# Performance work log

Hardware: AMD Instinct MI355X
Metric: run time of the kernel (lower is better)

The kernel has to match this reference:

```python
import jax, jax.numpy as jnp
import numpy as np

E = 8          # num_tasks / experts (world_size=1 -> local_experts=E)
N = 8192       # tokens
H = 768        # hidden_size
I = 3072       # intermediate_size
EPS = 1e-12    # layer_norm_eps


def setup_inputs() -> dict:
    key = jax.random.key(0)
    ks = jax.random.split(key, 8)
    x = jax.random.normal(ks[0], (N, H), dtype=jnp.float32)
    # arange task ids -> hash (mod E) gives perfectly balanced expert loads
    task_ids = jnp.arange(N, dtype=jnp.int64)
    s1 = 1.0 / np.sqrt(H)
    s2 = 1.0 / np.sqrt(I)
    W1 = jax.random.uniform(ks[1], (E, H, I), jnp.float32, -s1, s1)
    b1 = jax.random.uniform(ks[2], (E, I), jnp.float32, -s1, s1)
    W2 = jax.random.uniform(ks[3], (E, I, H), jnp.float32, -s2, s2)
    b2 = jax.random.uniform(ks[4], (E, H), jnp.float32, -s2, s2)
    gamma = jnp.ones((E, H), jnp.float32)
    beta = jnp.zeros((E, H), jnp.float32)
    return {"x": x, "task_ids": task_ids, "W1": W1, "b1": b1,
            "W2": W2, "b2": b2, "gamma": gamma, "beta": beta}


def reference(x, task_ids, W1, b1, W2, b2, gamma, beta):
    # hash protocol: expert = task_id % num_experts
    expert = (task_ids % E).astype(jnp.int32)
    order = jnp.argsort(expert)              # dispatch (scatter router)
    C = N // E                               # balanced capacity per expert
    xs = x[order].reshape(E, C, H)           # [E, C, H] per-expert token blocks
    # per-expert FFN as grouped GEMMs
    h = jnp.einsum('ech,ehi->eci', xs, W1) + b1[:, None, :]
    h = jax.nn.gelu(h, approximate=False)
    y = jnp.einsum('eci,eih->ech', h, W2) + b2[:, None, :]
    # dropout is identity in eval; residual + per-expert LayerNorm
    z = y + xs
    mu = jnp.mean(z, axis=-1, keepdims=True)
    var = jnp.mean((z - mu) ** 2, axis=-1, keepdims=True)
    z = (z - mu) * jax.lax.rsqrt(var + EPS)
    z = z * gamma[:, None, :] + beta[:, None, :]
    # combine (gather router): undo the dispatch permutation
    out = jnp.zeros((N, H), x.dtype).at[order].set(z.reshape(N, H))
    return out
```

## Files before the change

kernel.cpp:

```cpp
#include <hip/hip_runtime.h>
#include <hip/hip_bf16.h>

#define NE   8
#define NTOK 8192
#define DH   768
#define DI   3072
#define CAP  1024

typedef __bf16 bf16x8 __attribute__((ext_vector_type(8)));
typedef float  f32x4  __attribute__((ext_vector_type(4)));

__device__ __forceinline__ void gload_lds16(const void* g, void* l) {
  __builtin_amdgcn_global_load_lds(
      (const __attribute__((address_space(1))) unsigned int*)g,
      (__attribute__((address_space(3))) unsigned int*)l, 16, 0, 0);
}

__global__ __launch_bounds__(256)
void transpose_cvt(const float* __restrict__ in, __hip_bfloat16* __restrict__ out,
                   int R, int C) {
  __shared__ float tile[32][33];
  const int e = blockIdx.z;
  const float* src = in + (size_t)e * R * C;
  __hip_bfloat16* dst = out + (size_t)e * R * C;
  const int c0 = blockIdx.x * 32, r0 = blockIdx.y * 32;
  const int tx = threadIdx.x, ty = threadIdx.y;
#pragma unroll
  for (int j = 0; j < 4; ++j)
    tile[ty + 8 * j][tx] = src[(size_t)(r0 + ty + 8 * j) * C + c0 + tx];
  __syncthreads();
#pragma unroll
  for (int j = 0; j < 4; ++j)
    dst[(size_t)(c0 + ty + 8 * j) * R + r0 + tx] = __float2bfloat16(tile[tx][ty + 8 * j]);
}

__global__ __launch_bounds__(256)
void gather_cvt_x(const float* __restrict__ x, __hip_bfloat16* __restrict__ xs) {
  const int j = blockIdx.x * 256 + threadIdx.x;
  const int orow = j / 96;
  const int k8 = (j - orow * 96) * 8;
  const int e = orow >> 10, c = orow & 1023;
  const int tok = c * 8 + e;
  const float4* p = (const float4*)(x + (size_t)tok * DH + k8);
  float4 u = p[0], v = p[1];
  __hip_bfloat16 tmp[8];
  tmp[0] = __float2bfloat16(u.x); tmp[1] = __float2bfloat16(u.y);
  tmp[2] = __float2bfloat16(u.z); tmp[3] = __float2bfloat16(u.w);
  tmp[4] = __float2bfloat16(v.x); tmp[5] = __float2bfloat16(v.y);
  tmp[6] = __float2bfloat16(v.z); tmp[7] = __float2bfloat16(v.w);
  *(uint4*)(xs + (size_t)orow * DH + k8) = *(const uint4*)tmp;
}

template <int EPI>
__global__ __launch_bounds__(256)
void gemm_bt(const __hip_bfloat16* __restrict__ A,
             const __hip_bfloat16* __restrict__ Bt,
             const float* __restrict__ bias,
             void* __restrict__ OutP,
             int N, int K, int NK,
             size_t sAe, size_t sBe, size_t sOe, int sBias) {
  __shared__ __hip_bfloat16 As[128 * 64];
  __shared__ __hip_bfloat16 Bs[128 * 64];

  const int t = threadIdx.x;
  const int lane = t & 63;
  const int w = t >> 6;
  const int g = lane >> 4;
  const int l15 = lane & 15;
  const int wm = w >> 1, wn = w & 1;
  const int e = blockIdx.z;

  const __hip_bfloat16* Ae = A + (size_t)e * sAe + (size_t)blockIdx.y * 128 * K;
  const __hip_bfloat16* Be = Bt + (size_t)e * sBe + (size_t)blockIdx.x * 128 * K;

  const int rowStg = t >> 3;
  const int srcOff = ((t & 7) ^ (rowStg & 7)) * 8;
  const size_t stgBase = (size_t)rowStg * K + srcOff;

  f32x4 acc[4][4] = {};

  for (int kt = 0; kt < NK; ++kt) {
    const int k0 = kt * 64;
#pragma unroll
    for (int i = 0; i < 4; ++i) {
      gload_lds16(Ae + stgBase + (size_t)i * 32 * K + k0, (char*)As + (i * 256 + t) * 16);
      gload_lds16(Be + stgBase + (size_t)i * 32 * K + k0, (char*)Bs + (i * 256 + t) * 16);
    }
    __syncthreads();
#pragma unroll
    for (int ks = 0; ks < 2; ++ks) {
      bf16x8 af[4], bv[4];
#pragma unroll
      for (int fm = 0; fm < 4; ++fm) {
        const int r = wm * 64 + fm * 16 + l15;
        af[fm] = *(const bf16x8*)((const char*)As + r * 128 + ((ks * 4 + g) ^ (r & 7)) * 16);
      }
#pragma unroll
      for (int fn = 0; fn < 4; ++fn) {
        const int r = wn * 64 + fn * 16 + l15;
        bv[fn] = *(const bf16x8*)((const char*)Bs + r * 128 + ((ks * 4 + g) ^ (r & 7)) * 16);
      }
#pragma unroll
      for (int fm = 0; fm < 4; ++fm)
#pragma unroll
        for (int fn = 0; fn < 4; ++fn)
          acc[fm][fn] = __builtin_amdgcn_mfma_f32_16x16x32_bf16(af[fm], bv[fn], acc[fm][fn], 0, 0, 0);
    }
    __syncthreads();
  }

  const float* biasE = bias + (size_t)e * sBias + blockIdx.x * 128;
  if (EPI == 0) {
    __hip_bfloat16* O = (__hip_bfloat16*)OutP + (size_t)e * sOe +
                        (size_t)blockIdx.y * 128 * N + blockIdx.x * 128;
#pragma unroll
    for (int fm = 0; fm < 4; ++fm)
#pragma unroll
      for (int fn = 0; fn < 4; ++fn) {
        const int n = wn * 64 + fn * 16 + l15;
        const float bvv = biasE[n];
#pragma unroll
        for (int r = 0; r < 4; ++r) {
          const int m = wm * 64 + fm * 16 + g * 4 + r;
          float v = acc[fm][fn][r] + bvv;
          v = 0.5f * v * (1.0f + erff(v * 0.70710678118654752f));
          O[(size_t)m * N + n] = __float2bfloat16(v);
        }
      }
  } else {
    float* O = (float*)OutP + (size_t)e * sOe +
               (size_t)blockIdx.y * 128 * N + blockIdx.x * 128;
#pragma unroll
    for (int fm = 0; fm < 4; ++fm)
#pragma unroll
      for (int fn = 0; fn < 4; ++fn) {
        const int n = wn * 64 + fn * 16 + l15;
        const float bvv = biasE[n];
#pragma unroll
        for (int r = 0; r < 4; ++r) {
          const int m = wm * 64 + fm * 16 + g * 4 + r;
          O[(size_t)m * N + n] = acc[fm][fn][r] + bvv;
        }
      }
  }
}

__global__ __launch_bounds__(256)
void resid_ln(const float* __restrict__ y, const float* __restrict__ x,
              const float* __restrict__ gamma, const float* __restrict__ beta,
              float* __restrict__ out) {
  const int row = blockIdx.x;
  const int e = row >> 10, c = row & 1023;
  const int tok = c * 8 + e;
  const float* yr = y + (size_t)row * DH;
  const float* xr = x + (size_t)tok * DH;
  const int t = threadIdx.x;
  float z[3];
  float s = 0.f, s2 = 0.f;
#pragma unroll
  for (int j = 0; j < 3; ++j) {
    const float v = yr[t + 256 * j] + xr[t + 256 * j];
    z[j] = v; s += v; s2 += v * v;
  }
#pragma unroll
  for (int off = 32; off; off >>= 1) {
    s += __shfl_down(s, off);
    s2 += __shfl_down(s2, off);
  }
  __shared__ float rs[4], rs2[4];
  if ((t & 63) == 0) { rs[t >> 6] = s; rs2[t >> 6] = s2; }
  __syncthreads();
  const float S = rs[0] + rs[1] + rs[2] + rs[3];
  const float S2 = rs2[0] + rs2[1] + rs2[2] + rs2[3];
  const float mu = S * (1.0f / DH);
  const float var = S2 * (1.0f / DH) - mu * mu;
  const float rstd = rsqrtf(var + 1e-12f);
  const float* ga = gamma + (size_t)e * DH;
  const float* be = beta + (size_t)e * DH;
  float* orow = out + (size_t)tok * DH;
#pragma unroll
  for (int j = 0; j < 3; ++j) {
    const int h = t + 256 * j;
    orow[h] = (z[j] - mu) * rstd * ga[h] + be[h];
  }
}

extern "C" void kernel_launch(void* const* d_in, const int* in_sizes, int n_in,
                              void* d_out, int out_size, void* d_ws, size_t ws_size,
                              hipStream_t stream) {
  const float* x     = (const float*)d_in[0];
  const float* W1    = (const float*)d_in[2];
  const float* b1    = (const float*)d_in[3];
  const float* W2    = (const float*)d_in[4];
  const float* b2    = (const float*)d_in[5];
  const float* gamma = (const float*)d_in[6];
  const float* beta  = (const float*)d_in[7];
  float* out = (float*)d_out;

  __hip_bfloat16* W1t = (__hip_bfloat16*)d_ws;
  __hip_bfloat16* W2t = W1t + (size_t)NE * DH * DI;
  __hip_bfloat16* hbuf = W2t + (size_t)NE * DH * DI;
  __hip_bfloat16* xs = hbuf + (size_t)NTOK * DI;
  float* ybuf = (float*)xs;

  dim3 tb(32, 8);
  transpose_cvt<<<dim3(DI / 32, DH / 32, NE), tb, 0, stream>>>(W1, W1t, DH, DI);
  transpose_cvt<<<dim3(DH / 32, DI / 32, NE), tb, 0, stream>>>(W2, W2t, DI, DH);
  gather_cvt_x<<<(NTOK * (DH / 8)) / 256, 256, 0, stream>>>(x, xs);

  gemm_bt<0><<<dim3(DI / 128, CAP / 128, NE), 256, 0, stream>>>(
      xs, W1t, b1, hbuf, DI, DH, DH / 64,
      (size_t)CAP * DH, (size_t)DI * DH, (size_t)CAP * DI, DI);

  gemm_bt<1><<<dim3(DH / 128, CAP / 128, NE), 256, 0, stream>>>(
      hbuf, W2t, b2, ybuf, DH, DI, DI / 64,
      (size_t)CAP * DI, (size_t)DH * DI, (size_t)CAP * DH, DH);

  resid_ln<<<NTOK, 256, 0, stream>>>(ybuf, x, gamma, beta, out);
}
```

Measured before the change: 358.3 us.

## Split-K second GEMM, XCD-aware block remap, and vectorized swizzled weight transpose

```diff
diff --git a/kernel.cpp b/kernel.cpp
--- a/kernel.cpp
+++ b/kernel.cpp
@@ -19,19 +19,40 @@
 __global__ __launch_bounds__(256)
 void transpose_cvt(const float* __restrict__ in, __hip_bfloat16* __restrict__ out,
                    int R, int C) {
-  __shared__ float tile[32][33];
+  __shared__ float lds[64 * 64];
   const int e = blockIdx.z;
   const float* src = in + (size_t)e * R * C;
   __hip_bfloat16* dst = out + (size_t)e * R * C;
-  const int c0 = blockIdx.x * 32, r0 = blockIdx.y * 32;
-  const int tx = threadIdx.x, ty = threadIdx.y;
-#pragma unroll
-  for (int j = 0; j < 4; ++j)
-    tile[ty + 8 * j][tx] = src[(size_t)(r0 + ty + 8 * j) * C + c0 + tx];
+  const int c0 = blockIdx.x * 64, r0 = blockIdx.y * 64;
+  const int t = threadIdx.x;
+
+  {
+    const int rr = t >> 4;
+    const int cq = t & 15;
+#pragma unroll
+    for (int j = 0; j < 4; ++j) {
+      const int r = rr + 16 * j;
+      const float4 v = *(const float4*)(src + (size_t)(r0 + r) * C + c0 + cq * 4);
+      *(float4*)&lds[r * 64 + ((cq ^ ((r >> 3) & 7)) << 2)] = v;
+    }
+  }
   __syncthreads();
-#pragma unroll
-  for (int j = 0; j < 4; ++j)
-    dst[(size_t)(c0 + ty + 8 * j) * R + r0 + tx] = __float2bfloat16(tile[tx][ty + 8 * j]);
+  {
+    const int r8 = (t & 7) * 8;
+    const int cb = t >> 3;
+#pragma unroll
+    for (int j = 0; j < 2; ++j) {
+      const int c = cb + 32 * j;
+      __hip_bfloat16 tmp[8];
+#pragma unroll
+      for (int i = 0; i < 8; ++i) {
+        const int rr = r8 + i;
+        tmp[i] = __float2bfloat16(
+            lds[rr * 64 + ((((c >> 2) ^ ((rr >> 3) & 7)) << 2) | (c & 3))]);
+      }
+      *(uint4*)(dst + (size_t)(c0 + c) * R + r0 + r8) = *(const uint4*)tmp;
+    }
+  }
 }
 
 __global__ __launch_bounds__(256)
@@ -57,10 +78,21 @@
              const __hip_bfloat16* __restrict__ Bt,
              const float* __restrict__ bias,
              void* __restrict__ OutP,
-             int N, int K, int NK,
-             size_t sAe, size_t sBe, size_t sOe, int sBias) {
+             int N, int K, int KK, int gx, int gy, int nsplit,
+             size_t sAe, size_t sBe, size_t sOe, int sBias, size_t sSplit) {
   __shared__ __hip_bfloat16 As[128 * 64];
   __shared__ __hip_bfloat16 Bs[128 * 64];
+
+  const int nblk = gridDim.x;
+  const int chunk = nblk >> 3;
+  const int id = (blockIdx.x & 7) * chunk + (blockIdx.x >> 3);
+  const int per_e = gx * gy * nsplit;
+  const int e = id / per_e;
+  int r = id - e * per_e;
+  const int s = r / (gx * gy);
+  r -= s * (gx * gy);
+  const int bx = r / gy;
+  const int by = r - bx * gy;
 
   const int t = threadIdx.x;
   const int lane = t & 63;
@@ -68,10 +100,9 @@
   const int g = lane >> 4;
   const int l15 = lane & 15;
   const int wm = w >> 1, wn = w & 1;
-  const int e = blockIdx.z;
-
-  const __hip_bfloat16* Ae = A + (size_t)e * sAe + (size_t)blockIdx.y * 128 * K;
-  const __hip_bfloat16* Be = Bt + (size_t)e * sBe + (size_t)blockIdx.x * 128 * K;
+
+  const __hip_bfloat16* Ae = A + (size_t)e * sAe + (size_t)by * 128 * K;
+  const __hip_bfloat16* Be = Bt + (size_t)e * sBe + (size_t)bx * 128 * K;
 
   const int rowStg = t >> 3;
   const int srcOff = ((t & 7) ^ (rowStg & 7)) * 8;
@@ -79,8 +110,8 @@
 
   f32x4 acc[4][4] = {};
 
-  for (int kt = 0; kt < NK; ++kt) {
-    const int k0 = kt * 64;
+  for (int kt = 0; kt < KK; ++kt) {
+    const int k0 = (s * KK + kt) * 64;
 #pragma unroll
     for (int i = 0; i < 4; ++i) {
       gload_lds16(Ae + stgBase + (size_t)i * 32 * K + k0, (char*)As + (i * 256 + t) * 16);
@@ -92,13 +123,13 @@
       bf16x8 af[4], bv[4];
 #pragma unroll
       for (int fm = 0; fm < 4; ++fm) {
-        const int r = wm * 64 + fm * 16 + l15;
-        af[fm] = *(const bf16x8*)((const char*)As + r * 128 + ((ks * 4 + g) ^ (r & 7)) * 16);
+        const int rA = wm * 64 + fm * 16 + l15;
+        af[fm] = *(const bf16x8*)((const char*)As + rA * 128 + ((ks * 4 + g) ^ (rA & 7)) * 16);
       }
 #pragma unroll
       for (int fn = 0; fn < 4; ++fn) {
-        const int r = wn * 64 + fn * 16 + l15;
-        bv[fn] = *(const bf16x8*)((const char*)Bs + r * 128 + ((ks * 4 + g) ^ (r & 7)) * 16);
+        const int rB = wn * 64 + fn * 16 + l15;
+        bv[fn] = *(const bf16x8*)((const char*)Bs + rB * 128 + ((ks * 4 + g) ^ (rB & 7)) * 16);
       }
 #pragma unroll
       for (int fm = 0; fm < 4; ++fm)
@@ -109,10 +140,10 @@
     __syncthreads();
   }
 
-  const float* biasE = bias + (size_t)e * sBias + blockIdx.x * 128;
+  const float* biasE = bias + (size_t)e * sBias + bx * 128;
   if (EPI == 0) {
     __hip_bfloat16* O = (__hip_bfloat16*)OutP + (size_t)e * sOe +
-                        (size_t)blockIdx.y * 128 * N + blockIdx.x * 128;
+                        (size_t)by * 128 * N + bx * 128;
 #pragma unroll
     for (int fm = 0; fm < 4; ++fm)
 #pragma unroll
@@ -120,46 +151,49 @@
         const int n = wn * 64 + fn * 16 + l15;
         const float bvv = biasE[n];
 #pragma unroll
-        for (int r = 0; r < 4; ++r) {
-          const int m = wm * 64 + fm * 16 + g * 4 + r;
-          float v = acc[fm][fn][r] + bvv;
+        for (int rg = 0; rg < 4; ++rg) {
+          const int m = wm * 64 + fm * 16 + g * 4 + rg;
+          float v = acc[fm][fn][rg] + bvv;
           v = 0.5f * v * (1.0f + erff(v * 0.70710678118654752f));
           O[(size_t)m * N + n] = __float2bfloat16(v);
         }
       }
   } else {
-    float* O = (float*)OutP + (size_t)e * sOe +
-               (size_t)blockIdx.y * 128 * N + blockIdx.x * 128;
+    float* O = (float*)OutP + (size_t)s * sSplit + (size_t)e * sOe +
+               (size_t)by * 128 * N + bx * 128;
 #pragma unroll
     for (int fm = 0; fm < 4; ++fm)
 #pragma unroll
       for (int fn = 0; fn < 4; ++fn) {
         const int n = wn * 64 + fn * 16 + l15;
-        const float bvv = biasE[n];
-#pragma unroll
-        for (int r = 0; r < 4; ++r) {
-          const int m = wm * 64 + fm * 16 + g * 4 + r;
-          O[(size_t)m * N + n] = acc[fm][fn][r] + bvv;
+        const float bvv = (s == 0) ? biasE[n] : 0.0f;
+#pragma unroll
+        for (int rg = 0; rg < 4; ++rg) {
+          const int m = wm * 64 + fm * 16 + g * 4 + rg;
+          O[(size_t)m * N + n] = acc[fm][fn][rg] + bvv;
         }
       }
   }
 }
 
 __global__ __launch_bounds__(256)
-void resid_ln(const float* __restrict__ y, const float* __restrict__ x,
+void resid_ln(const float* __restrict__ y0, const float* __restrict__ y1, int two,
+              const float* __restrict__ x,
               const float* __restrict__ gamma, const float* __restrict__ beta,
               float* __restrict__ out) {
   const int row = blockIdx.x;
   const int e = row >> 10, c = row & 1023;
   const int tok = c * 8 + e;
-  const float* yr = y + (size_t)row * DH;
+  const float* y0r = y0 + (size_t)row * DH;
+  const float* y1r = y1 + (size_t)row * DH;
   const float* xr = x + (size_t)tok * DH;
   const int t = threadIdx.x;
   float z[3];
   float s = 0.f, s2 = 0.f;
 #pragma unroll
   for (int j = 0; j < 3; ++j) {
-    const float v = yr[t + 256 * j] + xr[t + 256 * j];
+    float v = y0r[t + 256 * j] + xr[t + 256 * j];
+    if (two) v += y1r[t + 256 * j];
     z[j] = v; s += v; s2 += v * v;
   }
 #pragma unroll
@@ -197,24 +231,26 @@
   const float* beta  = (const float*)d_in[7];
   float* out = (float*)d_out;
 
-  __hip_bfloat16* W1t = (__hip_bfloat16*)d_ws;
-  __hip_bfloat16* W2t = W1t + (size_t)NE * DH * DI;
-  __hip_bfloat16* hbuf = W2t + (size_t)NE * DH * DI;
-  __hip_bfloat16* xs = hbuf + (size_t)NTOK * DI;
-  float* ybuf = (float*)xs;
-
-  dim3 tb(32, 8);
-  transpose_cvt<<<dim3(DI / 32, DH / 32, NE), tb, 0, stream>>>(W1, W1t, DH, DI);
-  transpose_cvt<<<dim3(DH / 32, DI / 32, NE), tb, 0, stream>>>(W2, W2t, DI, DH);
+  char* base = (char*)d_ws;
+  __hip_bfloat16* W1t  = (__hip_bfloat16*)base;
+  __hip_bfloat16* W2t  = (__hip_bfloat16*)(base + 37748736ull);
+  __hip_bfloat16* hbuf = (__hip_bfloat16*)(base + 75497472ull);
+  __hip_bfloat16* xs   = (__hip_bfloat16*)(base + 125829120ull);
+  float* y0 = (float*)xs;
+  float* y1 = (float*)(base + 150994944ull);
+  const int nsplit = (ws_size >= 176160768ull) ? 2 : 1;
+
+  transpose_cvt<<<dim3(DI / 64, DH / 64, NE), 256, 0, stream>>>(W1, W1t, DH, DI);
+  transpose_cvt<<<dim3(DH / 64, DI / 64, NE), 256, 0, stream>>>(W2, W2t, DI, DH);
   gather_cvt_x<<<(NTOK * (DH / 8)) / 256, 256, 0, stream>>>(x, xs);
 
-  gemm_bt<0><<<dim3(DI / 128, CAP / 128, NE), 256, 0, stream>>>(
-      xs, W1t, b1, hbuf, DI, DH, DH / 64,
-      (size_t)CAP * DH, (size_t)DI * DH, (size_t)CAP * DI, DI);
-
-  gemm_bt<1><<<dim3(DH / 128, CAP / 128, NE), 256, 0, stream>>>(
-      hbuf, W2t, b2, ybuf, DH, DI, DI / 64,
-      (size_t)CAP * DI, (size_t)DH * DI, (size_t)CAP * DH, DH);
-
-  resid_ln<<<NTOK, 256, 0, stream>>>(ybuf, x, gamma, beta, out);
-}
+  gemm_bt<0><<<(DI / 128) * (CAP / 128) * NE, 256, 0, stream>>>(
+      xs, W1t, b1, hbuf, DI, DH, DH / 64, DI / 128, CAP / 128, 1,
+      (size_t)CAP * DH, (size_t)DI * DH, (size_t)CAP * DI, DI, 0);
+
+  gemm_bt<1><<<(DH / 128) * (CAP / 128) * NE * nsplit, 256, 0, stream>>>(
+      hbuf, W2t, b2, y0, DH, DI, DI / 64 / nsplit, DH / 128, CAP / 128, nsplit,
+      (size_t)CAP * DI, (size_t)DH * DI, (size_t)CAP * DH, DH, (size_t)NTOK * DH);
+
+  resid_ln<<<NTOK, 256, 0, stream>>>(y0, y1, nsplit - 1, x, gamma, beta, out);
+}
```

Result: faster. 349.7 us (-2.4%).
